# Performance work log

Measured on AMD Instinct MI355X. Metric: run time of the kernel, lower is better.

## Reference

```python
import jax, jax.numpy as jnp
import numpy as np

B, M, E, H, TOPK = 1024, 10000, 8, 512, 2


def setup_inputs() -> dict:
    key = jax.random.key(0)
    ks = jax.random.split(key, 6)
    s_in = 1.0 / np.sqrt(M)
    s_h = 1.0 / np.sqrt(H)
    x = jax.random.normal(ks[0], (B, M), dtype=jnp.float32)
    # Expert params, torch Linear layout stacked over experts
    W1 = jax.random.uniform(ks[1], (E, H, M), jnp.float32, -s_in, s_in)
    b1 = jax.random.uniform(ks[2], (E, H), jnp.float32, -s_in, s_in)
    W2 = jax.random.uniform(ks[3], (E, M, H), jnp.float32, -s_h, s_h)
    b2 = jax.random.uniform(ks[4], (E, M), jnp.float32, -s_h, s_h)
    Wr = jax.random.uniform(ks[5], (E, M), jnp.float32, -s_in, s_in)  # router, no bias
    return {"x": x, "W1": W1, "b1": b1, "W2": W2, "b2": b2, "Wr": Wr}


def reference(x, W1, b1, W2, b2, Wr):
    # Router: logits [B, E], sparse top-k softmax weights scattered to dense [B, E]
    logits = jnp.einsum('bm,em->be', x, Wr)
    topk_vals, topk_idx = jax.lax.top_k(logits, TOPK)
    probs = jax.nn.softmax(topk_vals, axis=-1)
    rw = jnp.zeros_like(logits).at[jnp.arange(B)[:, None], topk_idx].set(probs)
    # Dense all-expert MLP (faithful to original: every expert runs on every token)
    h = jax.nn.relu(jnp.einsum('bm,ehm->beh', x, W1) + b1)      # [B, E, H]
    eo = jnp.einsum('beh,emh->bem', h, W2) + b2                  # [B, E, M]
    # Masked weighted combine
    out = jnp.sum(rw[:, :, None] * eo, axis=1)                   # [B, M]
    return out
```

## Files before the change

### kernel.cpp

```cpp
#include <hip/hip_runtime.h>
#include <hip/hip_bf16.h>


#define B_TOK 1024
#define M_DIM 10000
#define E_NUM 8
#define H_DIM 512
#define NSTEP 313

typedef __attribute__((ext_vector_type(4))) float fx4;
typedef __attribute__((ext_vector_type(8))) short sx8;
typedef __attribute__((ext_vector_type(4))) short sx4;

#define LSTR 40
#define BUFS (256 * LSTR)

__device__ __forceinline__ short f2bf(float f) {
  union { __hip_bfloat16 h; short s; } u;
  u.h = __float2bfloat16(f);
  return u.s;
}

__device__ __forceinline__ sx8 pack8(fx4 a, fx4 b) {
  sx8 r;
  r[0] = f2bf(a[0]); r[1] = f2bf(a[1]); r[2] = f2bf(a[2]); r[3] = f2bf(a[3]);
  r[4] = f2bf(b[0]); r[5] = f2bf(b[1]); r[6] = f2bf(b[2]); r[7] = f2bf(b[3]);
  return r;
}

__device__ __forceinline__ void pipe_barrier() {
  asm volatile("s_waitcnt lgkmcnt(0)" ::: "memory");
  __builtin_amdgcn_sched_barrier(0);
  __builtin_amdgcn_s_barrier();
  __builtin_amdgcn_sched_barrier(0);
}

__global__ void k_zero(int* cnt, int* cnt2) {
  if (threadIdx.x < E_NUM) cnt[threadIdx.x] = 0;
  if (threadIdx.x < 2 * E_NUM) cnt2[threadIdx.x] = 0;
}

__global__ __launch_bounds__(256) void k_router(
    const float* __restrict__ x, const float* __restrict__ Wr,
    int* __restrict__ cnt, int* __restrict__ cnt2,
    int* __restrict__ tokAll, int* __restrict__ qlist2, float* __restrict__ wlist2)
{
  int b = blockIdx.x, t = threadIdx.x;
  const float* xr = x + (size_t)b * M_DIM;
  double acc[E_NUM];
#pragma unroll
  for (int e = 0; e < E_NUM; e++) acc[e] = 0.0;
  for (int m = t; m < M_DIM; m += 256) {
    float xv = xr[m];
#pragma unroll
    for (int e = 0; e < E_NUM; e++)
      acc[e] += (double)xv * (double)Wr[e * M_DIM + m];
  }
#pragma unroll
  for (int e = 0; e < E_NUM; e++) {
#pragma unroll
    for (int off = 32; off > 0; off >>= 1)
      acc[e] += __shfl_xor(acc[e], off);
  }
  __shared__ double part[4][E_NUM];
  int wave = t >> 6;
  if ((t & 63) == 0) {
    for (int e = 0; e < E_NUM; e++) part[wave][e] = acc[e];
  }
  __syncthreads();
  if (t == 0) {
    double lg[E_NUM];
    for (int e = 0; e < E_NUM; e++)
      lg[e] = part[0][e] + part[1][e] + part[2][e] + part[3][e];
    int i0 = 0;
    for (int e = 1; e < E_NUM; e++) if (lg[e] > lg[i0]) i0 = e;
    int i1 = (i0 == 0) ? 1 : 0;
    for (int e = 0; e < E_NUM; e++) if (e != i0 && lg[e] > lg[i1]) i1 = e;
    double ex = exp(lg[i1] - lg[i0]);
    float p0 = (float)(1.0 / (1.0 + ex));
    float p1 = (float)(ex / (1.0 + ex));
    int q0 = atomicAdd(&cnt[i0], 1);
    tokAll[i0 * B_TOK + q0] = b;
    int j0 = atomicAdd(&cnt2[i0 * 2 + 0], 1);
    qlist2[(i0 * 2 + 0) * B_TOK + j0] = q0;
    wlist2[(i0 * 2 + 0) * B_TOK + j0] = p0;
    int q1 = atomicAdd(&cnt[i1], 1);
    tokAll[i1 * B_TOK + q1] = b;
    int j1 = atomicAdd(&cnt2[i1 * 2 + 1], 1);
    qlist2[(i1 * 2 + 1) * B_TOK + j1] = q1;
    wlist2[(i1 * 2 + 1) * B_TOK + j1] = p1;
  }
}

#define M_MFMA(bo)                                                          \
  do {                                                                      \
    sx8 af[4], bfr[4];                                                      \
    _Pragma("unroll")                                                       \
    for (int m_ = 0; m_ < 4; m_++)                                          \
      af[m_] = *(const sx8*)(&SB[(bo) + (wr * 64 + m_ * 16 + lrow) * LSTR + khalf * 8]); \
    _Pragma("unroll")                                                       \
    for (int n_ = 0; n_ < 4; n_++)                                          \
      bfr[n_] = *(const sx8*)(&SB[(bo) + (128 + wc * 64 + n_ * 16 + lrow) * LSTR + khalf * 8]); \
    _Pragma("unroll")                                                       \
    for (int m_ = 0; m_ < 4; m_++)                                          \
      _Pragma("unroll")                                                     \
      for (int n_ = 0; n_ < 4; n_++)                                        \
        acc[m_][n_] = __builtin_amdgcn_mfma_f32_16x16x32_bf16(af[m_], bfr[n_], acc[m_][n_], 0, 0, 0); \
  } while (0)

__global__ __launch_bounds__(256) void k_mlp1(
    const float* __restrict__ x, const float* __restrict__ W1,
    const int* __restrict__ cnt, const int* __restrict__ tokAll,
    float* __restrict__ partials, int CH)
{
  int e = blockIdx.z;
  int tt = blockIdx.y >> 2, nt = blockIdx.y & 3;
  int kc = blockIdx.x;

  __shared__ int sh_ne, sh_eoff;
  __shared__ __align__(16) short SB[2 * BUFS];
  __shared__ int toks[128];

  int t = threadIdx.x;
  if (t == 0) {
    int off = 0;
    for (int k = 0; k < e; k++) off += cnt[k];
    sh_eoff = off; sh_ne = cnt[e];
  }
  __syncthreads();
  int ne = sh_ne, eoff = sh_eoff, row0 = tt * 128;
  if (row0 >= ne) return;
  int nvalid = min(128, ne - row0);

  if (t < 128) toks[t] = tokAll[e * B_TOK + row0 + min(t, nvalid - 1)];
  __syncthreads();

  int r4 = t >> 2, kch = t & 3;
  const float* xr0 = x + (size_t)toks[r4] * M_DIM;
  const float* xr1 = x + (size_t)toks[r4 + 64] * M_DIM;
  const float* wr0 = W1 + ((size_t)e * H_DIM + nt * 128 + r4) * M_DIM;
  const float* wr1 = W1 + ((size_t)e * H_DIM + nt * 128 + r4 + 64) * M_DIM;

  int lane = t & 63, wave = t >> 6;
  int wr = wave >> 1, wc = wave & 1;
  int lrow = lane & 15, khalf = lane >> 4;

  fx4 z4 = {0.f, 0.f, 0.f, 0.f};
  fx4 acc[4][4];
#pragma unroll
  for (int m = 0; m < 4; m++)
#pragma unroll
    for (int n = 0; n < 4; n++) acc[m][n] = z4;

  int s0 = kc * CH, s1 = min(s0 + CH, NSTEP);
  sx8 zv = {0, 0, 0, 0, 0, 0, 0, 0};

#define M1_LOAD(p, sN)                                                       \
  do {                                                                       \
    int off_ = (sN) * 32 + kch * 8;                                          \
    int oc_ = min(off_, M_DIM - 8);                                          \
    p##ok = (off_ + 8 <= M_DIM);                                             \
    p##A0 = *(const fx4*)(xr0 + oc_); p##A0b = *(const fx4*)(xr0 + oc_ + 4); \
    p##A1 = *(const fx4*)(xr1 + oc_); p##A1b = *(const fx4*)(xr1 + oc_ + 4); \
    p##B0 = *(const fx4*)(wr0 + oc_); p##B0b = *(const fx4*)(wr0 + oc_ + 4); \
    p##B1 = *(const fx4*)(wr1 + oc_); p##B1b = *(const fx4*)(wr1 + oc_ + 4); \
  } while (0)

#define M1_PACK(p, wo)                                                       \
  do {                                                                       \
    sx8 t0_ = p##ok ? pack8(p##A0, p##A0b) : zv;                             \
    sx8 t1_ = p##ok ? pack8(p##A1, p##A1b) : zv;                             \
    sx8 t2_ = p##ok ? pack8(p##B0, p##B0b) : zv;                             \
    sx8 t3_ = p##ok ? pack8(p##B1, p##B1b) : zv;                             \
    *(sx8*)(&SB[(wo) + r4 * LSTR + kch * 8]) = t0_;                          \
    *(sx8*)(&SB[(wo) + (r4 + 64) * LSTR + kch * 8]) = t1_;                   \
    *(sx8*)(&SB[(wo) + (128 + r4) * LSTR + kch * 8]) = t2_;                  \
    *(sx8*)(&SB[(wo) + (128 + r4 + 64) * LSTR + kch * 8]) = t3_;             \
  } while (0)

  fx4 pA0, pA0b, pA1, pA1b, pB0, pB0b, pB1, pB1b; bool pok;
  fx4 qA0, qA0b, qA1, qA1b, qB0, qB0b, qB1, qB1b; bool qok;

  M1_LOAD(p, s0);
  M1_PACK(p, 0);
  M1_LOAD(p, s0 + 1);
  M1_LOAD(q, s0 + 2);
  pipe_barrier();

  int c = 0, s = s0;
  while (s < s1) {
    M_MFMA(c * BUFS);
    if (s + 1 < s1) M1_PACK(p, (c ^ 1) * BUFS);
    if (s + 3 < s1) M1_LOAD(p, s + 3);
    pipe_barrier();
    c ^= 1; s++;
    if (s >= s1) break;
    M_MFMA(c * BUFS);
    if (s + 1 < s1) M1_PACK(q, (c ^ 1) * BUFS);
    if (s + 3 < s1) M1_LOAD(q, s + 3);
    pipe_barrier();
    c ^= 1; s++;
  }

#pragma unroll
  for (int m = 0; m < 4; m++)
#pragma unroll
    for (int n = 0; n < 4; n++) {
      int colg = nt * 128 + wc * 64 + n * 16 + lrow;
#pragma unroll
      for (int r = 0; r < 4; r++) {
        int rl = wr * 64 + m * 16 + khalf * 4 + r;
        if (rl < nvalid) {
          int grow = eoff + row0 + rl;
          partials[((size_t)kc * 2048 + grow) * H_DIM + colg] = acc[m][n][r];
        }
      }
    }
#undef M1_LOAD
#undef M1_PACK
}

__global__ __launch_bounds__(256) void k_hreduce(
    const float* __restrict__ partials, const float* __restrict__ b1,
    const int* __restrict__ cnt, short* __restrict__ hbuf, int KC)
{
  __shared__ int sc[E_NUM];
  int t = threadIdx.x;
  if (t < E_NUM) sc[t] = cnt[t];
  __syncthreads();
  int i = (blockIdx.x * 256 + t) * 4;
  int slot = i >> 9;
  int e = 0, off = 0;
  for (int k = 0; k < E_NUM - 1; k++) {
    if (slot >= off + sc[k]) { off += sc[k]; e++; } else break;
  }
  fx4 v = *(const fx4*)(partials + i);
  for (int kc = 1; kc < KC; kc++)
    v += *(const fx4*)(partials + (size_t)kc * 2048 * H_DIM + i);
  fx4 bv = *(const fx4*)(b1 + e * H_DIM + (i & (H_DIM - 1)));
  sx4 o;
#pragma unroll
  for (int j = 0; j < 4; j++) o[j] = f2bf(fmaxf(v[j] + bv[j], 0.f));
  *(sx4*)(hbuf + i) = o;
}

__global__ __launch_bounds__(256) void k_mlp2(
    const short* __restrict__ hbuf, const float* __restrict__ W2,
    const float* __restrict__ b2, const int* __restrict__ cnt,
    const int* __restrict__ cnt2, const int* __restrict__ tokAll,
    const int* __restrict__ qlist2, const float* __restrict__ wlist2,
    float* __restrict__ out, int ord)
{
  int e = blockIdx.z, mt = blockIdx.y, tt = blockIdx.x;

  __shared__ int sh_ne2, sh_eoff;
  __shared__ __align__(16) short SB[2 * BUFS];
  __shared__ int sl[128];
  __shared__ int tok2[128];
  __shared__ float wts[128];

  int t = threadIdx.x;
  if (t == 0) {
    int off = 0;
    for (int k = 0; k < e; k++) off += cnt[k];
    sh_eoff = off; sh_ne2 = cnt2[e * 2 + ord];
  }
  __syncthreads();
  int ne2 = sh_ne2, eoff = sh_eoff, row0 = tt * 128;
  if (row0 >= ne2) return;
  int nvalid = min(128, ne2 - row0);

  if (t < 128) {
    int j = row0 + min(t, nvalid - 1);
    int q = qlist2[(e * 2 + ord) * B_TOK + j];
    sl[t] = eoff + q;
    tok2[t] = tokAll[e * B_TOK + q];
    wts[t] = (t < nvalid) ? wlist2[(e * 2 + ord) * B_TOK + j] : 0.f;
  }
  __syncthreads();

  int r4 = t >> 2, kch = t & 3;
  const short* hr0 = hbuf + (size_t)sl[r4] * H_DIM;
  const short* hr1 = hbuf + (size_t)sl[r4 + 64] * H_DIM;
  const float* w20 = W2 + ((size_t)e * M_DIM + min(mt * 128 + r4, M_DIM - 1)) * H_DIM;
  const float* w21 = W2 + ((size_t)e * M_DIM + min(mt * 128 + r4 + 64, M_DIM - 1)) * H_DIM;

  int lane = t & 63, wave = t >> 6;
  int wr = wave >> 1, wc = wave & 1;
  int lrow = lane & 15, khalf = lane >> 4;

  fx4 z4 = {0.f, 0.f, 0.f, 0.f};
  fx4 acc[4][4];
#pragma unroll
  for (int m = 0; m < 4; m++)
#pragma unroll
    for (int n = 0; n < 4; n++) acc[m][n] = z4;

#define M2_LOAD(p, sN)                                                       \
  do {                                                                       \
    int off_ = (sN) * 32 + kch * 8;                                          \
    p##As0 = *(const sx8*)(hr0 + off_);                                      \
    p##As1 = *(const sx8*)(hr1 + off_);                                      \
    p##B0 = *(const fx4*)(w20 + off_); p##B0b = *(const fx4*)(w20 + off_ + 4); \
    p##B1 = *(const fx4*)(w21 + off_); p##B1b = *(const fx4*)(w21 + off_ + 4); \
  } while (0)

#define M2_PACK(p, wo)                                                       \
  do {                                                                       \
    sx8 t2_ = pack8(p##B0, p##B0b);                                          \
    sx8 t3_ = pack8(p##B1, p##B1b);                                          \
    *(sx8*)(&SB[(wo) + r4 * LSTR + kch * 8]) = p##As0;                       \
    *(sx8*)(&SB[(wo) + (r4 + 64) * LSTR + kch * 8]) = p##As1;                \
    *(sx8*)(&SB[(wo) + (128 + r4) * LSTR + kch * 8]) = t2_;                  \
    *(sx8*)(&SB[(wo) + (128 + r4 + 64) * LSTR + kch * 8]) = t3_;             \
  } while (0)

  sx8 pAs0, pAs1; fx4 pB0, pB0b, pB1, pB1b;
  sx8 qAs0, qAs1; fx4 qB0, qB0b, qB1, qB1b;

  M2_LOAD(p, 0);
  M2_PACK(p, 0);
  M2_LOAD(p, 1);
  M2_LOAD(q, 2);
  pipe_barrier();

  int c = 0, s = 0;
  while (s < 16) {
    M_MFMA(c * BUFS);
    if (s + 1 < 16) M2_PACK(p, (c ^ 1) * BUFS);
    if (s + 3 < 16) M2_LOAD(p, s + 3);
    pipe_barrier();
    c ^= 1; s++;
    if (s >= 16) break;
    M_MFMA(c * BUFS);
    if (s + 1 < 16) M2_PACK(q, (c ^ 1) * BUFS);
    if (s + 3 < 16) M2_LOAD(q, s + 3);
    pipe_barrier();
    c ^= 1; s++;
  }

#pragma unroll
  for (int m = 0; m < 4; m++)
#pragma unroll
    for (int n = 0; n < 4; n++) {
      int colg = mt * 128 + wc * 64 + n * 16 + lrow;
      if (colg < M_DIM) {
        float b2v = b2[(size_t)e * M_DIM + colg];
#pragma unroll
        for (int r = 0; r < 4; r++) {
          int rl = wr * 64 + m * 16 + khalf * 4 + r;
          if (rl < nvalid) {
            float v = wts[rl] * (acc[m][n][r] + b2v);
            float* dst = out + (size_t)tok2[rl] * M_DIM + colg;
            if (ord == 0) *dst = v;
            else *dst += v;
          }
        }
      }
    }
#undef M2_LOAD
#undef M2_PACK
}

extern "C" void kernel_launch(void* const* d_in, const int* in_sizes, int n_in,
                              void* d_out, int out_size, void* d_ws, size_t ws_size,
                              hipStream_t stream) {
  const float* x  = (const float*)d_in[0];
  const float* W1 = (const float*)d_in[1];
  const float* b1 = (const float*)d_in[2];
  const float* W2 = (const float*)d_in[3];
  const float* b2 = (const float*)d_in[4];
  const float* Wr = (const float*)d_in[5];
  float* out = (float*)d_out;

  int KC = (ws_size >= (size_t)36 * 1024 * 1024) ? 8 : 4;
  int CH = (NSTEP + KC - 1) / KC;

  char* p = (char*)d_ws;
  float* partials = (float*)p;        p += (size_t)KC * 2048 * H_DIM * 4;
  short* hbuf     = (short*)p;        p += (size_t)2048 * H_DIM * 2;
  int*   cnt      = (int*)p;          p += 64;
  int*   cnt2     = (int*)p;          p += 64;
  int*   tokAll   = (int*)p;          p += E_NUM * B_TOK * 4;
  int*   qlist2   = (int*)p;          p += 2 * E_NUM * B_TOK * 4;
  float* wlist2   = (float*)p;

  k_zero<<<1, 64, 0, stream>>>(cnt, cnt2);
  k_router<<<B_TOK, 256, 0, stream>>>(x, Wr, cnt, cnt2, tokAll, qlist2, wlist2);
  k_mlp1<<<dim3(KC, 12, E_NUM), 256, 0, stream>>>(x, W1, cnt, tokAll, partials, CH);
  k_hreduce<<<1024, 256, 0, stream>>>(partials, b1, cnt, hbuf, KC);
  k_mlp2<<<dim3(2, 79, E_NUM), 256, 0, stream>>>(hbuf, W2, b2, cnt, cnt2, tokAll,
                                                 qlist2, wlist2, out, 0);
  k_mlp2<<<dim3(2, 79, E_NUM), 256, 0, stream>>>(hbuf, W2, b2, cnt, cnt2, tokAll,
                                                 qlist2, wlist2, out, 1);
}
```

Measured before the change: 431.2 us.

## Pre-convert x and weights to bf16, stream tiles via global_load_lds triple buffer

Converts x to bf16 inside the router and adds a conversion kernel that writes W1 and W2 to bf16 in workspace before each GEMM. The GEMM kernels then copy global bf16 tiles straight into LDS with global_load_lds through a three-stage ring buffer, replacing register staging and in-loop packing, and raise MFMA priority with setprio. The goal is to cut register pressure and VALU conversion work in the main loops and overlap loads with compute. The cost is extra full passes over W1 and W2 (about 164MB fp32 read plus 82MB bf16 written per conversion), and KC is now fixed at 8, which assumes a large enough workspace.

```diff
diff --git a/kernel.cpp b/kernel.cpp
--- a/kernel.cpp
+++ b/kernel.cpp
@@ -12,9 +12,6 @@
 typedef __attribute__((ext_vector_type(8))) short sx8;
 typedef __attribute__((ext_vector_type(4))) short sx4;
 
-#define LSTR 40
-#define BUFS (256 * LSTR)
-
 __device__ __forceinline__ short f2bf(float f) {
   union { __hip_bfloat16 h; short s; } u;
   u.h = __float2bfloat16(f);
@@ -28,30 +25,52 @@
   return r;
 }
 
-__device__ __forceinline__ void pipe_barrier() {
-  asm volatile("s_waitcnt lgkmcnt(0)" ::: "memory");
-  __builtin_amdgcn_sched_barrier(0);
-  __builtin_amdgcn_s_barrier();
-  __builtin_amdgcn_sched_barrier(0);
-}
-
-__global__ void k_zero(int* cnt, int* cnt2) {
+__device__ __forceinline__ void gload16(const short* g, short* l) {
+  __builtin_amdgcn_global_load_lds(
+      (const __attribute__((address_space(1))) void*)g,
+      (__attribute__((address_space(3))) void*)l, 16, 0, 0);
+}
+
+#define PIPE_SYNC(VM)                                              \
+  do {                                                             \
+    asm volatile("s_waitcnt lgkmcnt(0)" ::: "memory");             \
+    __builtin_amdgcn_sched_barrier(0);                             \
+    asm volatile("s_waitcnt vmcnt(" #VM ")" ::: "memory");         \
+    __builtin_amdgcn_sched_barrier(0);                             \
+    __builtin_amdgcn_s_barrier();                                  \
+    __builtin_amdgcn_sched_barrier(0);                             \
+  } while (0)
+
+__global__ void k_zero(int* cnt, int* cnt2, int* zpad) {
   if (threadIdx.x < E_NUM) cnt[threadIdx.x] = 0;
   if (threadIdx.x < 2 * E_NUM) cnt2[threadIdx.x] = 0;
+  if (threadIdx.x < 16) zpad[threadIdx.x] = 0;
+}
+
+__global__ __launch_bounds__(256) void k_cvt(
+    const float* __restrict__ src, short* __restrict__ dst)
+{
+  size_t i = ((size_t)blockIdx.x * 256 + threadIdx.x) * 8;
+  fx4 a = *(const fx4*)(src + i);
+  fx4 b = *(const fx4*)(src + i + 4);
+  *(sx8*)(dst + i) = pack8(a, b);
 }
 
 __global__ __launch_bounds__(256) void k_router(
     const float* __restrict__ x, const float* __restrict__ Wr,
     int* __restrict__ cnt, int* __restrict__ cnt2,
-    int* __restrict__ tokAll, int* __restrict__ qlist2, float* __restrict__ wlist2)
+    int* __restrict__ tokAll, int* __restrict__ qlist2, float* __restrict__ wlist2,
+    short* __restrict__ xb)
 {
   int b = blockIdx.x, t = threadIdx.x;
   const float* xr = x + (size_t)b * M_DIM;
+  short* xbr = xb + (size_t)b * M_DIM;
   double acc[E_NUM];
 #pragma unroll
   for (int e = 0; e < E_NUM; e++) acc[e] = 0.0;
   for (int m = t; m < M_DIM; m += 256) {
     float xv = xr[m];
+    xbr[m] = f2bf(xv);
 #pragma unroll
     for (int e = 0; e < E_NUM; e++)
       acc[e] += (double)xv * (double)Wr[e * M_DIM + m];
@@ -92,33 +111,36 @@
   }
 }
 
-#define M_MFMA(bo)                                                          \
+#define M_MFMA3(cb)                                                         \
   do {                                                                      \
     sx8 af[4], bfr[4];                                                      \
     _Pragma("unroll")                                                       \
     for (int m_ = 0; m_ < 4; m_++)                                          \
-      af[m_] = *(const sx8*)(&SB[(bo) + (wr * 64 + m_ * 16 + lrow) * LSTR + khalf * 8]); \
+      af[m_] = *(const sx8*)(LA[cb] + (wr * 64 + m_ * 16 + lrow) * 32 + khalf * 8); \
     _Pragma("unroll")                                                       \
     for (int n_ = 0; n_ < 4; n_++)                                          \
-      bfr[n_] = *(const sx8*)(&SB[(bo) + (128 + wc * 64 + n_ * 16 + lrow) * LSTR + khalf * 8]); \
+      bfr[n_] = *(const sx8*)(LB[cb] + (wc * 64 + n_ * 16 + lrow) * 32 + khalf * 8); \
+    __builtin_amdgcn_s_setprio(1);                                          \
     _Pragma("unroll")                                                       \
     for (int m_ = 0; m_ < 4; m_++)                                          \
       _Pragma("unroll")                                                     \
       for (int n_ = 0; n_ < 4; n_++)                                        \
         acc[m_][n_] = __builtin_amdgcn_mfma_f32_16x16x32_bf16(af[m_], bfr[n_], acc[m_][n_], 0, 0, 0); \
+    __builtin_amdgcn_s_setprio(0);                                          \
   } while (0)
 
-__global__ __launch_bounds__(256) void k_mlp1(
-    const float* __restrict__ x, const float* __restrict__ W1,
+__global__ __launch_bounds__(256) void k_mlp1g(
+    const short* __restrict__ xb, const short* __restrict__ Wb,
     const int* __restrict__ cnt, const int* __restrict__ tokAll,
-    float* __restrict__ partials, int CH)
+    float* __restrict__ partials, const short* __restrict__ zpad, int CH)
 {
   int e = blockIdx.z;
   int tt = blockIdx.y >> 2, nt = blockIdx.y & 3;
   int kc = blockIdx.x;
 
   __shared__ int sh_ne, sh_eoff;
-  __shared__ __align__(16) short SB[2 * BUFS];
+  __shared__ __align__(16) short LA[3][4096];
+  __shared__ __align__(16) short LB[3][4096];
   __shared__ int toks[128];
 
   int t = threadIdx.x;
@@ -131,17 +153,19 @@
   int ne = sh_ne, eoff = sh_eoff, row0 = tt * 128;
   if (row0 >= ne) return;
   int nvalid = min(128, ne - row0);
-
   if (t < 128) toks[t] = tokAll[e * B_TOK + row0 + min(t, nvalid - 1)];
   __syncthreads();
 
-  int r4 = t >> 2, kch = t & 3;
-  const float* xr0 = x + (size_t)toks[r4] * M_DIM;
-  const float* xr1 = x + (size_t)toks[r4 + 64] * M_DIM;
-  const float* wr0 = W1 + ((size_t)e * H_DIM + nt * 128 + r4) * M_DIM;
-  const float* wr1 = W1 + ((size_t)e * H_DIM + nt * 128 + r4 + 64) * M_DIM;
-
   int lane = t & 63, wave = t >> 6;
+  int srow = wave * 32 + (lane >> 2);
+  int scol = (lane & 3) * 8;
+  const short* ap0 = xb + (size_t)toks[srow] * M_DIM + scol;
+  const short* ap1 = xb + (size_t)toks[srow + 16] * M_DIM + scol;
+  const short* bp0 = Wb + ((size_t)e * H_DIM + nt * 128 + srow) * M_DIM + scol;
+  const short* bp1 = bp0 + (size_t)16 * M_DIM;
+  int ld0 = (wave * 32) * 32;
+  int ld1 = (wave * 32 + 16) * 32;
+
   int wr = wave >> 1, wc = wave & 1;
   int lrow = lane & 15, khalf = lane >> 4;
 
@@ -153,53 +177,27 @@
     for (int n = 0; n < 4; n++) acc[m][n] = z4;
 
   int s0 = kc * CH, s1 = min(s0 + CH, NSTEP);
-  sx8 zv = {0, 0, 0, 0, 0, 0, 0, 0};
-
-#define M1_LOAD(p, sN)                                                       \
-  do {                                                                       \
-    int off_ = (sN) * 32 + kch * 8;                                          \
-    int oc_ = min(off_, M_DIM - 8);                                          \
-    p##ok = (off_ + 8 <= M_DIM);                                             \
-    p##A0 = *(const fx4*)(xr0 + oc_); p##A0b = *(const fx4*)(xr0 + oc_ + 4); \
-    p##A1 = *(const fx4*)(xr1 + oc_); p##A1b = *(const fx4*)(xr1 + oc_ + 4); \
-    p##B0 = *(const fx4*)(wr0 + oc_); p##B0b = *(const fx4*)(wr0 + oc_ + 4); \
-    p##B1 = *(const fx4*)(wr1 + oc_); p##B1b = *(const fx4*)(wr1 + oc_ + 4); \
+  int S = s1 - s0;
+
+#define STAGE1(buf, sN)                                        \
+  do {                                                         \
+    int ko_ = (sN) * 32;                                       \
+    bool ok_ = (ko_ + scol + 8 <= M_DIM);                      \
+    gload16(ok_ ? (ap0 + ko_) : zpad, LA[buf] + ld0);          \
+    gload16(ok_ ? (ap1 + ko_) : zpad, LA[buf] + ld1);          \
+    gload16(ok_ ? (bp0 + ko_) : zpad, LB[buf] + ld0);          \
+    gload16(ok_ ? (bp1 + ko_) : zpad, LB[buf] + ld1);          \
   } while (0)
 
-#define M1_PACK(p, wo)                                                       \
-  do {                                                                       \
-    sx8 t0_ = p##ok ? pack8(p##A0, p##A0b) : zv;                             \
-    sx8 t1_ = p##ok ? pack8(p##A1, p##A1b) : zv;                             \
-    sx8 t2_ = p##ok ? pack8(p##B0, p##B0b) : zv;                             \
-    sx8 t3_ = p##ok ? pack8(p##B1, p##B1b) : zv;                             \
-    *(sx8*)(&SB[(wo) + r4 * LSTR + kch * 8]) = t0_;                          \
-    *(sx8*)(&SB[(wo) + (r4 + 64) * LSTR + kch * 8]) = t1_;                   \
-    *(sx8*)(&SB[(wo) + (128 + r4) * LSTR + kch * 8]) = t2_;                  \
-    *(sx8*)(&SB[(wo) + (128 + r4 + 64) * LSTR + kch * 8]) = t3_;             \
-  } while (0)
-
-  fx4 pA0, pA0b, pA1, pA1b, pB0, pB0b, pB1, pB1b; bool pok;
-  fx4 qA0, qA0b, qA1, qA1b, qB0, qB0b, qB1, qB1b; bool qok;
-
-  M1_LOAD(p, s0);
-  M1_PACK(p, 0);
-  M1_LOAD(p, s0 + 1);
-  M1_LOAD(q, s0 + 2);
-  pipe_barrier();
-
-  int c = 0, s = s0;
-  while (s < s1) {
-    M_MFMA(c * BUFS);
-    if (s + 1 < s1) M1_PACK(p, (c ^ 1) * BUFS);
-    if (s + 3 < s1) M1_LOAD(p, s + 3);
-    pipe_barrier();
-    c ^= 1; s++;
-    if (s >= s1) break;
-    M_MFMA(c * BUFS);
-    if (s + 1 < s1) M1_PACK(q, (c ^ 1) * BUFS);
-    if (s + 3 < s1) M1_LOAD(q, s + 3);
-    pipe_barrier();
-    c ^= 1; s++;
+  STAGE1(0, s0);
+  STAGE1(1, s0 + 1);
+
+  for (int i = 0; i < S; i++) {
+    if (i + 1 < S) PIPE_SYNC(4);
+    else PIPE_SYNC(0);
+    int cb = i % 3;
+    if (i + 2 < S) STAGE1((i + 2) % 3, s0 + i + 2);
+    M_MFMA3(cb);
   }
 
 #pragma unroll
@@ -216,8 +214,7 @@
         }
       }
     }
-#undef M1_LOAD
-#undef M1_PACK
+#undef STAGE1
 }
 
 __global__ __launch_bounds__(256) void k_hreduce(
@@ -244,8 +241,8 @@
   *(sx4*)(hbuf + i) = o;
 }
 
-__global__ __launch_bounds__(256) void k_mlp2(
-    const short* __restrict__ hbuf, const float* __restrict__ W2,
+__global__ __launch_bounds__(256) void k_mlp2g(
+    const short* __restrict__ hbuf, const short* __restrict__ Wb,
     const float* __restrict__ b2, const int* __restrict__ cnt,
     const int* __restrict__ cnt2, const int* __restrict__ tokAll,
     const int* __restrict__ qlist2, const float* __restrict__ wlist2,
@@ -254,7 +251,8 @@
   int e = blockIdx.z, mt = blockIdx.y, tt = blockIdx.x;
 
   __shared__ int sh_ne2, sh_eoff;
-  __shared__ __align__(16) short SB[2 * BUFS];
+  __shared__ __align__(16) short LA[3][4096];
+  __shared__ __align__(16) short LB[3][4096];
   __shared__ int sl[128];
   __shared__ int tok2[128];
   __shared__ float wts[128];
@@ -279,13 +277,16 @@
   }
   __syncthreads();
 
-  int r4 = t >> 2, kch = t & 3;
-  const short* hr0 = hbuf + (size_t)sl[r4] * H_DIM;
-  const short* hr1 = hbuf + (size_t)sl[r4 + 64] * H_DIM;
-  const float* w20 = W2 + ((size_t)e * M_DIM + min(mt * 128 + r4, M_DIM - 1)) * H_DIM;
-  const float* w21 = W2 + ((size_t)e * M_DIM + min(mt * 128 + r4 + 64, M_DIM - 1)) * H_DIM;
-
   int lane = t & 63, wave = t >> 6;
+  int srow = wave * 32 + (lane >> 2);
+  int scol = (lane & 3) * 8;
+  const short* ap0 = hbuf + (size_t)sl[srow] * H_DIM + scol;
+  const short* ap1 = hbuf + (size_t)sl[srow + 16] * H_DIM + scol;
+  const short* bp0 = Wb + ((size_t)e * M_DIM + min(mt * 128 + srow, M_DIM - 1)) * H_DIM + scol;
+  const short* bp1 = Wb + ((size_t)e * M_DIM + min(mt * 128 + srow + 16, M_DIM - 1)) * H_DIM + scol;
+  int ld0 = (wave * 32) * 32;
+  int ld1 = (wave * 32 + 16) * 32;
+
   int wr = wave >> 1, wc = wave & 1;
   int lrow = lane & 15, khalf = lane >> 4;
 
@@ -296,47 +297,24 @@
 #pragma unroll
     for (int n = 0; n < 4; n++) acc[m][n] = z4;
 
-#define M2_LOAD(p, sN)                                                       \
-  do {                                                                       \
-    int off_ = (sN) * 32 + kch * 8;                                          \
-    p##As0 = *(const sx8*)(hr0 + off_);                                      \
-    p##As1 = *(const sx8*)(hr1 + off_);                                      \
-    p##B0 = *(const fx4*)(w20 + off_); p##B0b = *(const fx4*)(w20 + off_ + 4); \
-    p##B1 = *(const fx4*)(w21 + off_); p##B1b = *(const fx4*)(w21 + off_ + 4); \
+#define STAGE2(buf, sN)                          \
+  do {                                           \
+    int ko_ = (sN) * 32;                         \
+    gload16(ap0 + ko_, LA[buf] + ld0);           \
+    gload16(ap1 + ko_, LA[buf] + ld1);           \
+    gload16(bp0 + ko_, LB[buf] + ld0);           \
+    gload16(bp1 + ko_, LB[buf] + ld1);           \
   } while (0)
 
-#define M2_PACK(p, wo)                                                       \
-  do {                                                                       \
-    sx8 t2_ = pack8(p##B0, p##B0b);                                          \
-    sx8 t3_ = pack8(p##B1, p##B1b);                                          \
-    *(sx8*)(&SB[(wo) + r4 * LSTR + kch * 8]) = p##As0;                       \
-    *(sx8*)(&SB[(wo) + (r4 + 64) * LSTR + kch * 8]) = p##As1;                \
-    *(sx8*)(&SB[(wo) + (128 + r4) * LSTR + kch * 8]) = t2_;                  \
-    *(sx8*)(&SB[(wo) + (128 + r4 + 64) * LSTR + kch * 8]) = t3_;             \
-  } while (0)
-
-  sx8 pAs0, pAs1; fx4 pB0, pB0b, pB1, pB1b;
-  sx8 qAs0, qAs1; fx4 qB0, qB0b, qB1, qB1b;
-
-  M2_LOAD(p, 0);
-  M2_PACK(p, 0);
-  M2_LOAD(p, 1);
-  M2_LOAD(q, 2);
-  pipe_barrier();
-
-  int c = 0, s = 0;
-  while (s < 16) {
-    M_MFMA(c * BUFS);
-    if (s + 1 < 16) M2_PACK(p, (c ^ 1) * BUFS);
-    if (s + 3 < 16) M2_LOAD(p, s + 3);
-    pipe_barrier();
-    c ^= 1; s++;
-    if (s >= 16) break;
-    M_MFMA(c * BUFS);
-    if (s + 1 < 16) M2_PACK(q, (c ^ 1) * BUFS);
-    if (s + 3 < 16) M2_LOAD(q, s + 3);
-    pipe_barrier();
-    c ^= 1; s++;
+  STAGE2(0, 0);
+  STAGE2(1, 1);
+
+  for (int i = 0; i < 16; i++) {
+    if (i + 1 < 16) PIPE_SYNC(4);
+    else PIPE_SYNC(0);
+    int cb = i % 3;
+    if (i + 2 < 16) STAGE2((i + 2) % 3, i + 2);
+    M_MFMA3(cb);
   }
 
 #pragma unroll
@@ -358,8 +336,7 @@
         }
       }
     }
-#undef M2_LOAD
-#undef M2_PACK
+#undef STAGE2
 }
 
 extern "C" void kernel_launch(void* const* d_in, const int* in_sizes, int n_in,
@@ -373,8 +350,7 @@
   const float* Wr = (const float*)d_in[5];
   float* out = (float*)d_out;
 
-  int KC = (ws_size >= (size_t)36 * 1024 * 1024) ? 8 : 4;
-  int CH = (NSTEP + KC - 1) / KC;
+  const int KC = 8, CH = (NSTEP + KC - 1) / KC;
 
   char* p = (char*)d_ws;
   float* partials = (float*)p;        p += (size_t)KC * 2048 * H_DIM * 4;
@@ -383,14 +359,20 @@
   int*   cnt2     = (int*)p;          p += 64;
   int*   tokAll   = (int*)p;          p += E_NUM * B_TOK * 4;
   int*   qlist2   = (int*)p;          p += 2 * E_NUM * B_TOK * 4;
-  float* wlist2   = (float*)p;
-
-  k_zero<<<1, 64, 0, stream>>>(cnt, cnt2);
-  k_router<<<B_TOK, 256, 0, stream>>>(x, Wr, cnt, cnt2, tokAll, qlist2, wlist2);
-  k_mlp1<<<dim3(KC, 12, E_NUM), 256, 0, stream>>>(x, W1, cnt, tokAll, partials, CH);
+  float* wlist2   = (float*)p;        p += 2 * E_NUM * B_TOK * 4;
+  int*   zpad     = (int*)p;          p += 64;
+  short* xb       = (short*)p;        p += (size_t)B_TOK * M_DIM * 2;
+  short* Wb       = (short*)p;
+
+  k_zero<<<1, 64, 0, stream>>>(cnt, cnt2, zpad);
+  k_router<<<B_TOK, 256, 0, stream>>>(x, Wr, cnt, cnt2, tokAll, qlist2, wlist2, xb);
+  k_cvt<<<20000, 256, 0, stream>>>(W1, Wb);
+  k_mlp1g<<<dim3(KC, 12, E_NUM), 256, 0, stream>>>(xb, Wb, cnt, tokAll, partials,
+                                                   (const short*)zpad, CH);
   k_hreduce<<<1024, 256, 0, stream>>>(partials, b1, cnt, hbuf, KC);
-  k_mlp2<<<dim3(2, 79, E_NUM), 256, 0, stream>>>(hbuf, W2, b2, cnt, cnt2, tokAll,
-                                                 qlist2, wlist2, out, 0);
-  k_mlp2<<<dim3(2, 79, E_NUM), 256, 0, stream>>>(hbuf, W2, b2, cnt, cnt2, tokAll,
-                                                 qlist2, wlist2, out, 1);
-}
+  k_cvt<<<20000, 256, 0, stream>>>(W2, Wb);
+  k_mlp2g<<<dim3(2, 79, E_NUM), 256, 0, stream>>>(hbuf, Wb, b2, cnt, cnt2, tokAll,
+                                                  qlist2, wlist2, out, 0);
+  k_mlp2g<<<dim3(2, 79, E_NUM), 256, 0, stream>>>(hbuf, Wb, b2, cnt, cnt2, tokAll,
+                                                  qlist2, wlist2, out, 1);
+}
```

Result: faster. 376.6 us (-12.7%).
